# Kernel tuning notes

Hardware: AMD Instinct MI355X
Metric: run time of the kernel (lower is better)

## Reference

```python
import jax, jax.numpy as jnp
import numpy as np

HIDDEN = 2048
HEADS = 16
KV_HEADS = 1
HEAD_DIM = 128
SEQ = 2048
BATCH = 1
LAM = 0.5


def _rotate_half(x):
    h = x.shape[-1] // 2
    return jnp.concatenate([-x[..., h:], x[..., :h]], axis=-1)


def _apply_rope(t, cos, sin):
    # t: [B,S,H,D], cos/sin: [S,D] -> broadcast over batch & heads
    c = cos[None, :, None, :]
    s = sin[None, :, None, :]
    return t * c + _rotate_half(t) * s


def setup_inputs() -> dict:
    key = jax.random.key(0)
    ks = jax.random.split(key, 8)
    x = jax.random.normal(ks[0], (BATCH, SEQ, HIDDEN), dtype=jnp.float32)
    # realistic RoPE tables, rotate-half layout: [S, D]
    inv_freq = 1.0 / (10000.0 ** (np.arange(0, HEAD_DIM, 2, dtype=np.float32) / HEAD_DIM))
    t = np.arange(SEQ, dtype=np.float32)
    ang = np.outer(t, inv_freq)                      # [S, D/2]
    ang = np.concatenate([ang, ang], axis=-1)        # [S, D]
    freqs_cos = jnp.asarray(np.cos(ang))
    freqs_sin = jnp.asarray(np.sin(ang))
    mask = jnp.tril(jnp.ones((SEQ, SEQ), dtype=bool))  # causal, True = attend
    scale = 1.0 / np.sqrt(HIDDEN)
    q1_w = jax.random.normal(ks[1], (HIDDEN, HEADS * HEAD_DIM), dtype=jnp.float32) * scale
    q2_w = jax.random.normal(ks[2], (HIDDEN, HEADS * HEAD_DIM), dtype=jnp.float32) * scale
    k_w = jax.random.normal(ks[3], (HIDDEN, KV_HEADS * HEAD_DIM), dtype=jnp.float32) * scale
    v_w = jax.random.normal(ks[4], (HIDDEN, KV_HEADS * HEAD_DIM), dtype=jnp.float32) * scale
    out_w = jax.random.normal(ks[5], (HEADS * HEAD_DIM, HIDDEN), dtype=jnp.float32) * scale
    return {"x": x, "freqs_cos": freqs_cos, "freqs_sin": freqs_sin, "mask": mask,
            "q1_w": q1_w, "q2_w": q2_w, "k_w": k_w, "v_w": v_w, "out_w": out_w}


def reference(x, freqs_cos, freqs_sin, mask, q1_w, q2_w, k_w, v_w, out_w):
    B, S, _ = x.shape
    q1 = (x @ q1_w).reshape(B, S, HEADS, HEAD_DIM)
    q2 = (x @ q2_w).reshape(B, S, HEADS, HEAD_DIM)
    k = (x @ k_w).reshape(B, S, KV_HEADS, HEAD_DIM)
    v = (x @ v_w).reshape(B, S, KV_HEADS, HEAD_DIM)
    q1 = _apply_rope(q1, freqs_cos, freqs_sin)
    q2 = _apply_rope(q2, freqs_cos, freqs_sin)
    k = _apply_rope(k, freqs_cos, freqs_sin)
    # MQA broadcast of the single KV head
    k = jnp.repeat(k, HEADS // KV_HEADS, axis=2)  # [B,S,H,D]
    v = jnp.repeat(v, HEADS // KV_HEADS, axis=2)
    inv_sqrt_d = 1.0 / jnp.sqrt(jnp.float32(HEAD_DIM))
    s1 = jnp.einsum('bqhd,bkhd->bhqk', q1, k) * inv_sqrt_d
    s2 = jnp.einsum('bqhd,bkhd->bhqk', q2, k) * inv_sqrt_d
    m = mask[None, None, :, :]
    neg = jnp.float32(-1e10)
    s1 = jnp.where(m, s1, neg)
    s2 = jnp.where(m, s2, neg)
    a1 = jax.nn.softmax(s1, axis=-1)
    a2 = jax.nn.softmax(s2, axis=-1)
    a = a1 - LAM * a2
    a = a / (jnp.sum(a, axis=-1, keepdims=True) + 1e-8)
    a = jnp.maximum(a, 0.0)
    out = jnp.einsum('bhqk,bkhd->bqhd', a, v).reshape(B, S, HEADS * HEAD_DIM)
    return out @ out_w
```

## Files before the change

### kernel.cpp

```cpp
#include <hip/hip_runtime.h>
#include <hip/hip_bf16.h>

typedef __attribute__((ext_vector_type(8))) short bf16x8;
typedef __attribute__((ext_vector_type(4))) float f32x4;

#define MFMA16(a, b, c) __builtin_amdgcn_mfma_f32_16x16x32_bf16((a), (b), (c), 0, 0, 0)

#define LDQ 4352
#define KSCALE 0.12751743f

__device__ __forceinline__ ushort f2bf(float f) {
    unsigned int x = __float_as_uint(f);
    x += 0x7fffu + ((x >> 16) & 1u);
    return (ushort)(x >> 16);
}
__device__ __forceinline__ float bf2f(ushort u) {
    return __uint_as_float(((unsigned int)u) << 16);
}
__device__ __forceinline__ float exp2_fast(float x) {
    float r;
    asm("v_exp_f32 %0, %1" : "=v"(r) : "v"(x));
    return r;
}
__device__ __forceinline__ unsigned int cvtpk(float lo, float hi) {
    unsigned int r;
    asm("v_cvt_pk_bf16_f32 %0, %1, %2" : "=v"(r) : "v"(lo), "v"(hi));
    return r;
}

__device__ __forceinline__ void gload16(const ushort* g, ushort* l) {
    __builtin_amdgcn_global_load_lds((const __attribute__((address_space(1))) unsigned int*)g,
                                     (__attribute__((address_space(3))) unsigned int*)l, 16, 0, 0);
}

__global__ __launch_bounds__(256) void prep_k(const float* __restrict__ x, ushort* __restrict__ xb,
                                              const float* __restrict__ q1w, const float* __restrict__ q2w,
                                              const float* __restrict__ kw, const float* __restrict__ vw,
                                              const float* __restrict__ ow,
                                              ushort* __restrict__ w1t, ushort* __restrict__ w2t,
                                              ushort* __restrict__ wkt, ushort* __restrict__ wvt,
                                              ushort* __restrict__ wot) {
    int bid = blockIdx.x;
    if (bid < 4096) {
        int i = bid * 256 + threadIdx.x;
        float4 v = ((const float4*)x)[i];
        ushort4 u;
        u.x = f2bf(v.x); u.y = f2bf(v.y); u.z = f2bf(v.z); u.w = f2bf(v.w);
        ((ushort4*)xb)[i] = u;
        return;
    }
    bid -= 4096;
    const float* in;
    ushort* out;
    int C, TX;
    if (bid < 4096) { in = q1w; out = w1t; C = 2048; TX = 64; }
    else if (bid < 8192) { bid -= 4096; in = q2w; out = w2t; C = 2048; TX = 64; }
    else if (bid < 12288) { bid -= 8192; in = ow; out = wot; C = 2048; TX = 64; }
    else if (bid < 12544) { bid -= 12288; in = kw; out = wkt; C = 128; TX = 4; }
    else { bid -= 12544; in = vw; out = wvt; C = 128; TX = 4; }
    __shared__ ushort t[32][33];
    const int c0 = (bid % TX) * 32, r0 = (bid / TX) * 32;
    const int lx = threadIdx.x & 31, ly = threadIdx.x >> 5;
#pragma unroll
    for (int i = 0; i < 4; ++i)
        t[ly + i * 8][lx] = f2bf(in[(size_t)(r0 + ly + i * 8) * C + c0 + lx]);
    __syncthreads();
#pragma unroll
    for (int i = 0; i < 4; ++i)
        out[(size_t)(c0 + ly + i * 8) * 2048 + r0 + lx] = t[lx][ly + i * 8];
}

__global__ __launch_bounds__(256) void rope_vt_k(ushort* __restrict__ qkv, const float* __restrict__ cs,
                                                 const float* __restrict__ sn, ushort* __restrict__ vtb) {
    int bid = blockIdx.x;
    if (bid < 16896) {
        int i = bid * 256 + threadIdx.x;
        int d = i & 63;
        int rest = i >> 6;
        int s = rest / 33;
        int h = rest - s * 33;
        size_t base = (size_t)s * LDQ + h * 128;
        float t0 = bf2f(qkv[base + d]);
        float t1 = bf2f(qkv[base + d + 64]);
        float cA = cs[s * 128 + d], cB = cs[s * 128 + d + 64];
        float sA = sn[s * 128 + d], sB = sn[s * 128 + d + 64];
        qkv[base + d] = f2bf(t0 * cA - t1 * sA);
        qkv[base + d + 64] = f2bf(t1 * cB + t0 * sB);
        return;
    }
    bid -= 16896;
    __shared__ ushort t[32][33];
    const ushort* in = qkv + 4224;
    const int c0 = (bid & 3) * 32, r0 = (bid >> 2) * 32;
    const int lx = threadIdx.x & 31, ly = threadIdx.x >> 5;
#pragma unroll
    for (int i = 0; i < 4; ++i)
        t[ly + i * 8][lx] = in[(size_t)(r0 + ly + i * 8) * LDQ + c0 + lx];
    __syncthreads();
#pragma unroll
    for (int i = 0; i < 4; ++i)
        vtb[(size_t)(c0 + ly + i * 8) * 2048 + r0 + lx] = t[lx][ly + i * 8];
}

__global__ __launch_bounds__(256) void gemm_glds_k(const ushort* __restrict__ A, int lda,
                                                   const ushort* __restrict__ Bt, int ldb,
                                                   void* __restrict__ C, int ldc,
                                                   int K, int nbx, int cbf, int kst) {
    __shared__ ushort As[2][128 * 32];
    __shared__ ushort Bs[2][128 * 32];
    const int tid = threadIdx.x;
    const int lane = tid & 63, wid = tid >> 6;
    const int cpx = (int)gridDim.x >> 3;
    const int swz = ((int)blockIdx.x & 7) * cpx + ((int)blockIdx.x >> 3);
    const int nt = swz / nbx;
    const int m0 = (swz % nbx) * 128, n0 = nt * 128;
    const int wr = wid >> 1, wc = wid & 1;
    const int l15 = lane & 15, lhi = lane >> 4;
    const float cscale = (nt == kst) ? KSCALE : 1.0f;

    const int srow0 = wid * 32 + (lane >> 2);
    const int srow1 = srow0 + 16;
    const int scol = (((lane & 3) ^ ((lane >> 3) & 3)) << 3);
    const ushort* gA0 = A + (size_t)(m0 + srow0) * lda + scol;
    const ushort* gA1 = A + (size_t)(m0 + srow1) * lda + scol;
    const ushort* gB0 = Bt + (size_t)(n0 + srow0) * ldb + scol;
    const ushort* gB1 = Bt + (size_t)(n0 + srow1) * ldb + scol;
    const int seg0 = (wid * 2 + 0) * 512, seg1 = (wid * 2 + 1) * 512;

    f32x4 acc[4][4];
#pragma unroll
    for (int m = 0; m < 4; ++m)
#pragma unroll
        for (int n = 0; n < 4; ++n) acc[m][n] = (f32x4){0.f, 0.f, 0.f, 0.f};

    const int rsw = ((l15 >> 1) & 3) << 4;
    const int fcol = (lhi << 4) ^ rsw;

    gload16(gA0, &As[0][seg0]);
    gload16(gA1, &As[0][seg1]);
    gload16(gB0, &Bs[0][seg0]);
    gload16(gB1, &Bs[0][seg1]);
    __syncthreads();

    int cur = 0;
    for (int k0 = 0; k0 < K; k0 += 32) {
        if (k0 + 32 < K) {
            gload16(gA0 + k0 + 32, &As[cur ^ 1][seg0]);
            gload16(gA1 + k0 + 32, &As[cur ^ 1][seg1]);
            gload16(gB0 + k0 + 32, &Bs[cur ^ 1][seg0]);
            gload16(gB1 + k0 + 32, &Bs[cur ^ 1][seg1]);
        }
        const char* aB = (const char*)As[cur];
        const char* bB = (const char*)Bs[cur];
        bf16x8 af[4], bfr[4];
#pragma unroll
        for (int m = 0; m < 4; ++m)
            af[m] = *(const bf16x8*)(aB + (wr * 64 + m * 16 + l15) * 64 + fcol);
#pragma unroll
        for (int n = 0; n < 4; ++n)
            bfr[n] = *(const bf16x8*)(bB + (wc * 64 + n * 16 + l15) * 64 + fcol);
#pragma unroll
        for (int m = 0; m < 4; ++m)
#pragma unroll
            for (int n = 0; n < 4; ++n)
                acc[m][n] = MFMA16(af[m], bfr[n], acc[m][n]);
        __syncthreads();
        cur ^= 1;
    }

#pragma unroll
    for (int m = 0; m < 4; ++m) {
        const int rb = m0 + wr * 64 + m * 16 + lhi * 4;
#pragma unroll
        for (int n = 0; n < 4; ++n) {
            const int col = n0 + wc * 64 + n * 16 + l15;
#pragma unroll
            for (int r = 0; r < 4; ++r) {
                float v = acc[m][n][r] * cscale;
                if (cbf)
                    ((ushort*)C)[(size_t)(rb + r) * ldc + col] = f2bf(v);
                else
                    ((float*)C)[(size_t)(rb + r) * ldc + col] = v;
            }
        }
    }
}


__device__ __forceinline__ void stage_k_chunk(const ushort* __restrict__ kb, int kc,
                                              ushort* __restrict__ kbuf, int wid, int lane) {
#pragma unroll
    for (int u = 0; u < 2; ++u) {
        const int w = wid * 2 + u;
        const int row = w * 4 + (lane >> 4);
        const int colb = ((lane & 15) * 16) ^ ((row & 7) << 4);
        gload16(kb + (size_t)(kc + row) * LDQ + (colb >> 1), kbuf + w * 512);
    }
}

__device__ __forceinline__ void stage_v_chunk(const ushort* __restrict__ vtb, int kc,
                                              ushort* __restrict__ vbuf, int wid, int lane) {
#pragma unroll
    for (int u = 0; u < 2; ++u) {
        const int w = wid * 2 + u;
        const int rowd = w * 16 + (lane >> 2);
        const int colb = ((lane & 3) * 16) ^ (((rowd >> 1) & 3) << 4);
        gload16(vtb + (size_t)rowd * 2048 + kc + (colb >> 1), vbuf + w * 512);
    }
}

__device__ __forceinline__ void load_k_frags(const ushort* __restrict__ kbuf, int l15, int lhi,
                                             bf16x8 kf[2][4]) {
    const char* kB = (const char*)kbuf;
#pragma unroll
    for (int n2 = 0; n2 < 2; ++n2) {
        const int r = n2 * 16 + l15;
#pragma unroll
        for (int c = 0; c < 4; ++c)
            kf[n2][c] = *(const bf16x8*)(kB + r * 256 + ((lhi * 16 + c * 64) ^ ((r & 7) << 4)));
    }
}

template <bool MASKED>
__device__ __forceinline__ void sums_chunk(const ushort* __restrict__ kbuf, int kc,
                                           int l15, int lhi, int qrow,
                                           const bf16x8* q1f, const bf16x8* q2f,
                                           float& sum1, float& sum2) {
    bf16x8 kf[2][4];
    load_k_frags(kbuf, l15, lhi, kf);
    f32x4 s1[2], s2[2];
#pragma unroll
    for (int n2 = 0; n2 < 2; ++n2) {
        s1[n2] = (f32x4){0.f, 0.f, 0.f, 0.f};
        s2[n2] = (f32x4){0.f, 0.f, 0.f, 0.f};
#pragma unroll
        for (int c = 0; c < 4; ++c) {
            s1[n2] = MFMA16(kf[n2][c], q1f[c], s1[n2]);
            s2[n2] = MFMA16(kf[n2][c], q2f[c], s2[n2]);
        }
    }
    const int kbase = kc + lhi * 4;
#pragma unroll
    for (int n2 = 0; n2 < 2; ++n2)
#pragma unroll
        for (int r = 0; r < 4; ++r) {
            float e1 = exp2_fast(s1[n2][r]);
            float e2 = exp2_fast(s2[n2][r]);
            if (MASKED) {
                bool ok = (kbase + n2 * 16 + r) <= qrow;
                e1 = ok ? e1 : 0.f;
                e2 = ok ? e2 : 0.f;
            }
            sum1 += e1;
            sum2 += e2;
        }
}

__global__ __launch_bounds__(256) void attn_sums_k(const ushort* __restrict__ qkv,
                                                   float* __restrict__ sums) {
    __shared__ ushort Kbuf[2 * 4096];
    const int bid = blockIdx.x;
    const int strip = 127 - (bid >> 3);
    const int cs = (bid >> 2) & 1;
    const int hg = bid & 3;
    const int q0 = strip << 4;
    const int lane = threadIdx.x & 63, wid = threadIdx.x >> 6;
    const int h = hg * 4 + wid;
    const int l15 = lane & 15, lhi = lane >> 4;
    const int qrow = q0 + l15;
    const ushort* kb = qkv + 4096;

    bf16x8 q1f[4], q2f[4];
    {
        size_t base = (size_t)qrow * LDQ + h * 128 + lhi * 8;
#pragma unroll
        for (int c = 0; c < 4; ++c) {
            q1f[c] = *(const bf16x8*)(qkv + base + c * 32);
            q2f[c] = *(const bf16x8*)(qkv + base + 2048 + c * 32);
        }
    }

    const int nchunk = (strip >> 1) + 1;
    const int ndiag = nchunk - 1;
    const int nch = (nchunk - cs + 1) >> 1;

    float sum1 = 0.f, sum2 = 0.f;
    if (nch > 0) stage_k_chunk(kb, cs * 32, Kbuf, wid, lane);
    __syncthreads();
    for (int i = 0; i < nch; ++i) {
        const int ch = cs + 2 * i, kc = ch << 5;
        if (i + 1 < nch) stage_k_chunk(kb, kc + 64, Kbuf + ((i + 1) & 1) * 4096, wid, lane);
        const ushort* kcur = Kbuf + (i & 1) * 4096;
        if (ch == ndiag)
            sums_chunk<true>(kcur, kc, l15, lhi, qrow, q1f, q2f, sum1, sum2);
        else
            sums_chunk<false>(kcur, kc, l15, lhi, qrow, q1f, q2f, sum1, sum2);
        __syncthreads();
    }

    sum1 += __shfl_xor(sum1, 16);
    sum1 += __shfl_xor(sum1, 32);
    sum2 += __shfl_xor(sum2, 16);
    sum2 += __shfl_xor(sum2, 32);

    if (lhi == 0) {
        sums[(size_t)((cs * 2 + 0) * 16 + h) * 2048 + qrow] = sum1;
        sums[(size_t)((cs * 2 + 1) * 16 + h) * 2048 + qrow] = sum2;
    }
}

template <bool MASKED>
__device__ __forceinline__ void pv_chunk(const ushort* __restrict__ kbuf, const ushort* __restrict__ vbuf,
                                         int kc, ushort* __restrict__ Pb,
                                         int l15, int lhi, int qrow,
                                         const bf16x8* q1f, const bf16x8* q2f,
                                         float c1, float c2, f32x4* o) {
    bf16x8 kf[2][4];
    load_k_frags(kbuf, l15, lhi, kf);
    bf16x8 vf[8];
    const char* vB = (const char*)vbuf;
#pragma unroll
    for (int dt = 0; dt < 8; ++dt) {
        const int d = dt * 16 + l15;
        vf[dt] = *(const bf16x8*)(vB + d * 64 + ((lhi * 16) ^ (((d >> 1) & 3) << 4)));
    }
    f32x4 s1[2], s2[2];
#pragma unroll
    for (int n2 = 0; n2 < 2; ++n2) {
        s1[n2] = (f32x4){0.f, 0.f, 0.f, 0.f};
        s2[n2] = (f32x4){0.f, 0.f, 0.f, 0.f};
#pragma unroll
        for (int c = 0; c < 4; ++c) {
            s1[n2] = MFMA16(kf[n2][c], q1f[c], s1[n2]);
            s2[n2] = MFMA16(kf[n2][c], q2f[c], s2[n2]);
        }
    }
    const int kbase = kc + lhi * 4;
#pragma unroll
    for (int n2 = 0; n2 < 2; ++n2) {
        float p[4];
#pragma unroll
        for (int r = 0; r < 4; ++r) {
            float e1 = exp2_fast(s1[n2][r]) * c1;
            float e2 = exp2_fast(s2[n2][r]) * c2;
            float pv = fmaxf(e1 - e2, 0.f);
            if (MASKED) pv = ((kbase + n2 * 16 + r) <= qrow) ? pv : 0.f;
            p[r] = pv;
        }
        uint2 w;
        w.x = cvtpk(p[0], p[1]);
        w.y = cvtpk(p[2], p[3]);
        *(uint2*)(Pb + l15 * 40 + n2 * 16 + lhi * 4) = w;
    }
    asm volatile("s_waitcnt lgkmcnt(0)" ::: "memory");
    bf16x8 pf = *(const bf16x8*)(Pb + l15 * 40 + lhi * 8);
#pragma unroll
    for (int dt = 0; dt < 8; ++dt)
        o[dt] = MFMA16(pf, vf[dt], o[dt]);
}

__global__ __launch_bounds__(256) void attn_pv_k(const ushort* __restrict__ qkv,
                                                 const ushort* __restrict__ vtb,
                                                 const float* __restrict__ sums,
                                                 ushort* __restrict__ op0,
                                                 ushort* __restrict__ op1) {
    __shared__ ushort Kbuf[2 * 4096];
    __shared__ ushort Vbuf[2 * 4096];
    __shared__ ushort P[4][16][40];
    const int bid = blockIdx.x;
    const int strip = 127 - (bid >> 3);
    const int cs = (bid >> 2) & 1;
    const int hg = bid & 3;
    const int q0 = strip << 4;
    const int lane = threadIdx.x & 63, wid = threadIdx.x >> 6;
    const int h = hg * 4 + wid;
    const int l15 = lane & 15, lhi = lane >> 4;
    const int qrow = q0 + l15;
    const ushort* kb = qkv + 4096;

    bf16x8 q1f[4], q2f[4];
    {
        size_t base = (size_t)qrow * LDQ + h * 128 + lhi * 8;
#pragma unroll
        for (int c = 0; c < 4; ++c) {
            q1f[c] = *(const bf16x8*)(qkv + base + c * 32);
            q2f[c] = *(const bf16x8*)(qkv + base + 2048 + c * 32);
        }
    }

    const float sum1 = sums[(size_t)(0 * 16 + h) * 2048 + qrow] + sums[(size_t)(2 * 16 + h) * 2048 + qrow];
    const float sum2 = sums[(size_t)(1 * 16 + h) * 2048 + qrow] + sums[(size_t)(3 * 16 + h) * 2048 + qrow];
    const float inv_denom = 1.0f / (0.5f + 1e-8f);
    const float c1 = inv_denom / sum1;
    const float c2 = 0.5f * inv_denom / sum2;

    f32x4 o[8];
#pragma unroll
    for (int dt = 0; dt < 8; ++dt) o[dt] = (f32x4){0.f, 0.f, 0.f, 0.f};

    const int nchunk = (strip >> 1) + 1;
    const int ndiag = nchunk - 1;
    const int nch = (nchunk - cs + 1) >> 1;

    if (nch > 0) {
        stage_k_chunk(kb, cs * 32, Kbuf, wid, lane);
        stage_v_chunk(vtb, cs * 32, Vbuf, wid, lane);
    }
    __syncthreads();
    for (int i = 0; i < nch; ++i) {
        const int ch = cs + 2 * i, kc = ch << 5;
        if (i + 1 < nch) {
            stage_k_chunk(kb, kc + 64, Kbuf + ((i + 1) & 1) * 4096, wid, lane);
            stage_v_chunk(vtb, kc + 64, Vbuf + ((i + 1) & 1) * 4096, wid, lane);
        }
        const ushort* kcur = Kbuf + (i & 1) * 4096;
        const ushort* vcur = Vbuf + (i & 1) * 4096;
        ushort* Pb = &P[wid][0][0];
        if (ch == ndiag)
            pv_chunk<true>(kcur, vcur, kc, Pb, l15, lhi, qrow, q1f, q2f, c1, c2, o);
        else
            pv_chunk<false>(kcur, vcur, kc, Pb, l15, lhi, qrow, q1f, q2f, c1, c2, o);
        __syncthreads();
    }

    ushort* op = cs ? op1 : op0;
#pragma unroll
    for (int dt = 0; dt < 8; ++dt)
#pragma unroll
        for (int r = 0; r < 4; ++r)
            op[(size_t)(q0 + lhi * 4 + r) * 2048 + h * 128 + dt * 16 + l15] = f2bf(o[dt][r]);
}

__device__ __forceinline__ unsigned int addbf2(unsigned int a, unsigned int b) {
    float alo = bf2f((ushort)a), ahi = bf2f((ushort)(a >> 16));
    float blo = bf2f((ushort)b), bhi = bf2f((ushort)(b >> 16));
    return (unsigned int)f2bf(alo + blo) | ((unsigned int)f2bf(ahi + bhi) << 16);
}
__global__ void combine_k(const ushort* __restrict__ o0, const ushort* __restrict__ o1,
                          ushort* __restrict__ out, int n8) {
    int i = blockIdx.x * blockDim.x + threadIdx.x;
    if (i >= n8) return;
    uint4 a = ((const uint4*)o0)[i];
    uint4 b = ((const uint4*)o1)[i];
    uint4 c;
    c.x = addbf2(a.x, b.x);
    c.y = addbf2(a.y, b.y);
    c.z = addbf2(a.z, b.z);
    c.w = addbf2(a.w, b.w);
    ((uint4*)out)[i] = c;
}

extern "C" void kernel_launch(void* const* d_in, const int* in_sizes, int n_in,
                              void* d_out, int out_size, void* d_ws, size_t ws_size,
                              hipStream_t stream) {
    const int S = 2048, HID = 2048;

    const float* x = (const float*)d_in[0];
    const float* fcos = (const float*)d_in[1];
    const float* fsin = (const float*)d_in[2];
    const float* q1w = (const float*)d_in[4];
    const float* q2w = (const float*)d_in[5];
    const float* kw = (const float*)d_in[6];
    const float* vw = (const float*)d_in[7];
    const float* ow = (const float*)d_in[8];

    ushort* xb = (ushort*)d_ws;
    ushort* btq = xb + (size_t)4194304;
    ushort* w1t = btq;
    ushort* w2t = btq + (size_t)2048 * 2048;
    ushort* wkt = btq + (size_t)4096 * 2048;
    ushort* wvt = btq + (size_t)4224 * 2048;
    ushort* wot = btq + (size_t)8912896;
    ushort* qkvb = wot + (size_t)4194304;
    ushort* vtb = qkvb + (size_t)8912896;
    float* sums = (float*)(vtb + (size_t)262144);
    ushort* opart0 = xb;
    ushort* opart1 = w1t;
    ushort* aob = w2t;

    prep_k<<<dim3(16896), dim3(256), 0, stream>>>(x, xb, q1w, q2w, kw, vw, ow,
                                                  w1t, w2t, wkt, wvt, wot);

    gemm_glds_k<<<dim3(544), dim3(256), 0, stream>>>(xb, HID, btq, HID, qkvb, LDQ, HID, 16, 1, 32);

    rope_vt_k<<<dim3(17152), dim3(256), 0, stream>>>(qkvb, fcos, fsin, vtb);

    attn_sums_k<<<dim3(1024), dim3(256), 0, stream>>>(qkvb, sums);

    attn_pv_k<<<dim3(1024), dim3(256), 0, stream>>>(qkvb, vtb, sums, opart0, opart1);

    combine_k<<<dim3(2048), dim3(256), 0, stream>>>(opart0, opart1, aob, S * HID / 8);

    gemm_glds_k<<<dim3(256), dim3(256), 0, stream>>>(aob, HID, wot, HID, (float*)d_out, HID, HID, 16, 0, -1);
}
```

Measured before the change: 196.0 us.

## Fuse RoPE and V transpose into QKV GEMM epilogue with 8-wave tiles

The separate RoPE/V-transpose kernel is removed. The QKV projection GEMM now applies rotary embedding (plus the K scale) in its epilogue and writes V transposed directly. The GEMM is also restructured to 512 threads (8 waves, each owning a 64x32 slice), with each wave's N columns split so that d and d+64 land in the same thread for the RoPE pair. This saves a full read/write pass over the QKV buffer and a kernel launch, at the cost of strided epilogue stores and more register and occupancy pressure per block.

```diff
diff --git a/kernel.cpp b/kernel.cpp
--- a/kernel.cpp
+++ b/kernel.cpp
@@ -70,117 +70,114 @@
         out[(size_t)(c0 + ly + i * 8) * 2048 + r0 + lx] = t[lx][ly + i * 8];
 }
 
-__global__ __launch_bounds__(256) void rope_vt_k(ushort* __restrict__ qkv, const float* __restrict__ cs,
-                                                 const float* __restrict__ sn, ushort* __restrict__ vtb) {
-    int bid = blockIdx.x;
-    if (bid < 16896) {
-        int i = bid * 256 + threadIdx.x;
-        int d = i & 63;
-        int rest = i >> 6;
-        int s = rest / 33;
-        int h = rest - s * 33;
-        size_t base = (size_t)s * LDQ + h * 128;
-        float t0 = bf2f(qkv[base + d]);
-        float t1 = bf2f(qkv[base + d + 64]);
-        float cA = cs[s * 128 + d], cB = cs[s * 128 + d + 64];
-        float sA = sn[s * 128 + d], sB = sn[s * 128 + d + 64];
-        qkv[base + d] = f2bf(t0 * cA - t1 * sA);
-        qkv[base + d + 64] = f2bf(t1 * cB + t0 * sB);
-        return;
-    }
-    bid -= 16896;
-    __shared__ ushort t[32][33];
-    const ushort* in = qkv + 4224;
-    const int c0 = (bid & 3) * 32, r0 = (bid >> 2) * 32;
-    const int lx = threadIdx.x & 31, ly = threadIdx.x >> 5;
-#pragma unroll
-    for (int i = 0; i < 4; ++i)
-        t[ly + i * 8][lx] = in[(size_t)(r0 + ly + i * 8) * LDQ + c0 + lx];
-    __syncthreads();
-#pragma unroll
-    for (int i = 0; i < 4; ++i)
-        vtb[(size_t)(c0 + ly + i * 8) * 2048 + r0 + lx] = t[lx][ly + i * 8];
-}
-
-__global__ __launch_bounds__(256) void gemm_glds_k(const ushort* __restrict__ A, int lda,
-                                                   const ushort* __restrict__ Bt, int ldb,
-                                                   void* __restrict__ C, int ldc,
-                                                   int K, int nbx, int cbf, int kst) {
-    __shared__ ushort As[2][128 * 32];
-    __shared__ ushort Bs[2][128 * 32];
+template <bool FUSE>
+__global__ __launch_bounds__(512) void gemm8_k(const ushort* __restrict__ A, int lda,
+                                               const ushort* __restrict__ Bt, int ldb,
+                                               void* __restrict__ C, int ldc,
+                                               int K, int nbx, int cbf,
+                                               const float* __restrict__ cs,
+                                               const float* __restrict__ sn,
+                                               ushort* __restrict__ vtb) {
+    __shared__ ushort As[2 * 4096];
+    __shared__ ushort Bs[2 * 4096];
     const int tid = threadIdx.x;
     const int lane = tid & 63, wid = tid >> 6;
     const int cpx = (int)gridDim.x >> 3;
     const int swz = ((int)blockIdx.x & 7) * cpx + ((int)blockIdx.x >> 3);
     const int nt = swz / nbx;
     const int m0 = (swz % nbx) * 128, n0 = nt * 128;
-    const int wr = wid >> 1, wc = wid & 1;
+    const int wr = wid >> 2, wc = wid & 3;
     const int l15 = lane & 15, lhi = lane >> 4;
-    const float cscale = (nt == kst) ? KSCALE : 1.0f;
-
-    const int srow0 = wid * 32 + (lane >> 2);
-    const int srow1 = srow0 + 16;
-    const int scol = (((lane & 3) ^ ((lane >> 3) & 3)) << 3);
-    const ushort* gA0 = A + (size_t)(m0 + srow0) * lda + scol;
-    const ushort* gA1 = A + (size_t)(m0 + srow1) * lda + scol;
-    const ushort* gB0 = Bt + (size_t)(n0 + srow0) * ldb + scol;
-    const ushort* gB1 = Bt + (size_t)(n0 + srow1) * ldb + scol;
-    const int seg0 = (wid * 2 + 0) * 512, seg1 = (wid * 2 + 1) * 512;
-
-    f32x4 acc[4][4];
+
+    const int srow = tid >> 2;
+    const int scol = (((tid & 3) ^ ((srow >> 1) & 3)) << 3);
+    const ushort* gA = A + (size_t)(m0 + srow) * lda + scol;
+    const ushort* gB = Bt + (size_t)(n0 + srow) * ldb + scol;
+    ushort* lA = &As[wid * 512];
+    ushort* lB = &Bs[wid * 512];
+
+    f32x4 acc[4][2];
 #pragma unroll
     for (int m = 0; m < 4; ++m)
 #pragma unroll
-        for (int n = 0; n < 4; ++n) acc[m][n] = (f32x4){0.f, 0.f, 0.f, 0.f};
-
-    const int rsw = ((l15 >> 1) & 3) << 4;
-    const int fcol = (lhi << 4) ^ rsw;
-
-    gload16(gA0, &As[0][seg0]);
-    gload16(gA1, &As[0][seg1]);
-    gload16(gB0, &Bs[0][seg0]);
-    gload16(gB1, &Bs[0][seg1]);
+        for (int n = 0; n < 2; ++n) acc[m][n] = (f32x4){0.f, 0.f, 0.f, 0.f};
+
+    const int fcol = (lhi << 4) ^ (((l15 >> 1) & 3) << 4);
+
+    gload16(gA, lA);
+    gload16(gB, lB);
     __syncthreads();
 
     int cur = 0;
     for (int k0 = 0; k0 < K; k0 += 32) {
         if (k0 + 32 < K) {
-            gload16(gA0 + k0 + 32, &As[cur ^ 1][seg0]);
-            gload16(gA1 + k0 + 32, &As[cur ^ 1][seg1]);
-            gload16(gB0 + k0 + 32, &Bs[cur ^ 1][seg0]);
-            gload16(gB1 + k0 + 32, &Bs[cur ^ 1][seg1]);
-        }
-        const char* aB = (const char*)As[cur];
-        const char* bB = (const char*)Bs[cur];
-        bf16x8 af[4], bfr[4];
+            gload16(gA + k0 + 32, lA + (cur ^ 1) * 4096);
+            gload16(gB + k0 + 32, lB + (cur ^ 1) * 4096);
+        }
+        const char* aB = (const char*)&As[cur * 4096];
+        const char* bB = (const char*)&Bs[cur * 4096];
+        bf16x8 af[4], bfr[2];
 #pragma unroll
         for (int m = 0; m < 4; ++m)
             af[m] = *(const bf16x8*)(aB + (wr * 64 + m * 16 + l15) * 64 + fcol);
 #pragma unroll
-        for (int n = 0; n < 4; ++n)
-            bfr[n] = *(const bf16x8*)(bB + (wc * 64 + n * 16 + l15) * 64 + fcol);
+        for (int n = 0; n < 2; ++n)
+            bfr[n] = *(const bf16x8*)(bB + (wc * 16 + n * 64 + l15) * 64 + fcol);
 #pragma unroll
         for (int m = 0; m < 4; ++m)
 #pragma unroll
-            for (int n = 0; n < 4; ++n)
+            for (int n = 0; n < 2; ++n)
                 acc[m][n] = MFMA16(af[m], bfr[n], acc[m][n]);
         __syncthreads();
         cur ^= 1;
     }
 
-#pragma unroll
-    for (int m = 0; m < 4; ++m) {
-        const int rb = m0 + wr * 64 + m * 16 + lhi * 4;
-#pragma unroll
-        for (int n = 0; n < 4; ++n) {
-            const int col = n0 + wc * 64 + n * 16 + l15;
-#pragma unroll
-            for (int r = 0; r < 4; ++r) {
-                float v = acc[m][n][r] * cscale;
-                if (cbf)
-                    ((ushort*)C)[(size_t)(rb + r) * ldc + col] = f2bf(v);
-                else
-                    ((float*)C)[(size_t)(rb + r) * ldc + col] = v;
+    if (FUSE) {
+        if (nt == 33) {
+#pragma unroll
+            for (int m = 0; m < 4; ++m) {
+                const int rb = m0 + wr * 64 + m * 16 + lhi * 4;
+#pragma unroll
+                for (int n = 0; n < 2; ++n) {
+                    const int d = wc * 16 + n * 64 + l15;
+                    uint2 w;
+                    w.x = cvtpk(acc[m][n][0], acc[m][n][1]);
+                    w.y = cvtpk(acc[m][n][2], acc[m][n][3]);
+                    *(uint2*)(vtb + (size_t)d * 2048 + rb) = w;
+                }
+            }
+        } else {
+            const float scale = (nt == 32) ? KSCALE : 1.0f;
+            ushort* out = (ushort*)C;
+            const int d0 = wc * 16 + l15;
+#pragma unroll
+            for (int m = 0; m < 4; ++m) {
+                const int rb = m0 + wr * 64 + m * 16 + lhi * 4;
+#pragma unroll
+                for (int r = 0; r < 4; ++r) {
+                    const int row = rb + r;
+                    float c0 = cs[row * 128 + d0], c1 = cs[row * 128 + d0 + 64];
+                    float s0 = sn[row * 128 + d0], s1 = sn[row * 128 + d0 + 64];
+                    float t0 = acc[m][0][r], t1 = acc[m][1][r];
+                    out[(size_t)row * ldc + n0 + d0] = f2bf((t0 * c0 - t1 * s0) * scale);
+                    out[(size_t)row * ldc + n0 + d0 + 64] = f2bf((t1 * c1 + t0 * s1) * scale);
+                }
+            }
+        }
+    } else {
+#pragma unroll
+        for (int m = 0; m < 4; ++m) {
+            const int rb = m0 + wr * 64 + m * 16 + lhi * 4;
+#pragma unroll
+            for (int n = 0; n < 2; ++n) {
+                const int col = n0 + wc * 16 + n * 64 + l15;
+#pragma unroll
+                for (int r = 0; r < 4; ++r) {
+                    if (cbf)
+                        ((ushort*)C)[(size_t)(rb + r) * ldc + col] = f2bf(acc[m][n][r]);
+                    else
+                        ((float*)C)[(size_t)(rb + r) * ldc + col] = acc[m][n][r];
+                }
             }
         }
     }
@@ -481,9 +478,8 @@
     prep_k<<<dim3(16896), dim3(256), 0, stream>>>(x, xb, q1w, q2w, kw, vw, ow,
                                                   w1t, w2t, wkt, wvt, wot);
 
-    gemm_glds_k<<<dim3(544), dim3(256), 0, stream>>>(xb, HID, btq, HID, qkvb, LDQ, HID, 16, 1, 32);
-
-    rope_vt_k<<<dim3(17152), dim3(256), 0, stream>>>(qkvb, fcos, fsin, vtb);
+    gemm8_k<true><<<dim3(544), dim3(512), 0, stream>>>(xb, HID, btq, HID, qkvb, LDQ, HID, 16, 1,
+                                                       fcos, fsin, vtb);
 
     attn_sums_k<<<dim3(1024), dim3(256), 0, stream>>>(qkvb, sums);
 
@@ -491,5 +487,6 @@
 
     combine_k<<<dim3(2048), dim3(256), 0, stream>>>(opart0, opart1, aob, S * HID / 8);
 
-    gemm_glds_k<<<dim3(256), dim3(256), 0, stream>>>(aob, HID, wot, HID, (float*)d_out, HID, HID, 16, 0, -1);
-}
+    gemm8_k<false><<<dim3(256), dim3(512), 0, stream>>>(aob, HID, wot, HID, (float*)d_out, HID, HID, 16, 0,
+                                                        nullptr, nullptr, nullptr);
+}
```

Result: faster. 179.3 us (-8.5%).
